# Kernel tuning notes

Hardware: AMD Instinct MI355X
Metric: run time of the kernel (lower is better)

Reference implementation:

```python
import jax, jax.numpy as jnp
import numpy as np

B, S, D = 4, 2048, 768
H = 12
DH = D // H
FF = 4 * D
EPS = 1e-5


def _layernorm(x, g, b):
    mu = jnp.mean(x, axis=-1, keepdims=True)
    var = jnp.mean(jnp.square(x - mu), axis=-1, keepdims=True)
    return (x - mu) * jax.lax.rsqrt(var + EPS) * g + b


def setup_inputs() -> dict:
    key = jax.random.key(0)
    ks = jax.random.split(key, 16)
    s_d = 1.0 / np.sqrt(D)
    s_ff = 1.0 / np.sqrt(FF)
    inp = {
        "x": jax.random.normal(ks[0], (B, S, D), jnp.float32),
        # LayerNorm 1
        "ln1_g": jnp.ones((D,), jnp.float32),
        "ln1_b": jnp.zeros((D,), jnp.float32),
        # attention linears (stored as [in, out], i.e. already transposed)
        "Wq": jax.random.normal(ks[1], (D, D), jnp.float32) * s_d,
        "bq": jax.random.normal(ks[2], (D,), jnp.float32) * s_d,
        "Wk": jax.random.normal(ks[3], (D, D), jnp.float32) * s_d,
        "bk": jax.random.normal(ks[4], (D,), jnp.float32) * s_d,
        "Wv": jax.random.normal(ks[5], (D, D), jnp.float32) * s_d,
        "bv": jax.random.normal(ks[6], (D,), jnp.float32) * s_d,
        "Wo": jax.random.normal(ks[7], (D, D), jnp.float32) * s_d,
        "bo": jax.random.normal(ks[8], (D,), jnp.float32) * s_d,
        # LayerNorm 2
        "ln2_g": jnp.ones((D,), jnp.float32),
        "ln2_b": jnp.zeros((D,), jnp.float32),
        # feed-forward (bias always on, per torch code)
        "W1": jax.random.normal(ks[9], (D, FF), jnp.float32) * s_d,
        "b1": jax.random.normal(ks[10], (FF,), jnp.float32) * s_d,
        "W2": jax.random.normal(ks[11], (FF, D), jnp.float32) * s_ff,
        "b2": jax.random.normal(ks[12], (D,), jnp.float32) * s_ff,
    }
    return inp


def reference(x, ln1_g, ln1_b, Wq, bq, Wk, bk, Wv, bv, Wo, bo,
              ln2_g, ln2_b, W1, b1, W2, b2):
    # --- attention branch (pre-LN) ---
    h = _layernorm(x, ln1_g, ln1_b)
    q = (h @ Wq + bq).reshape(B, S, H, DH).transpose(0, 2, 1, 3)  # [B,H,S,DH]
    k = (h @ Wk + bk).reshape(B, S, H, DH).transpose(0, 2, 1, 3)
    v = (h @ Wv + bv).reshape(B, S, H, DH).transpose(0, 2, 1, 3)
    scores = jnp.einsum("bhqd,bhkd->bhqk", q, k) / np.sqrt(DH)
    causal = jnp.tril(jnp.ones((S, S), bool))
    scores = jnp.where(causal, scores, -jnp.inf)
    attn = jax.nn.softmax(scores, axis=-1)
    out = jnp.einsum("bhqk,bhkd->bhqd", attn, v)
    out = out.transpose(0, 2, 1, 3).reshape(B, S, D)
    x = x + (out @ Wo + bo)
    # --- feed-forward branch (pre-LN, exact GELU) ---
    h2 = _layernorm(x, ln2_g, ln2_b)
    ff = jax.nn.gelu(h2 @ W1 + b1, approximate=False) @ W2 + b2
    return x + ff
```

## Files before the change

kernel.cpp:

```cpp
#include <hip/hip_runtime.h>
#include <math.h>

#define B_ 4
#define S_ 2048
#define D_ 768
#define H_ 12
#define DH_ 64
#define FF_ 3072

using short8  = __attribute__((ext_vector_type(8))) short;
using f32x4   = __attribute__((ext_vector_type(4))) float;
using f32x16  = __attribute__((ext_vector_type(16))) float;
using float4v = __attribute__((ext_vector_type(4))) float;
using ushort4v= __attribute__((ext_vector_type(4))) unsigned short;

__device__ __forceinline__ unsigned short f2bf(float f) {
  unsigned u = __builtin_bit_cast(unsigned, f);
  u += 0x7FFFu + ((u >> 16) & 1u);
  return (unsigned short)(u >> 16);
}

__device__ __forceinline__ unsigned cvt_pk_bf16(float a, float b) {
  unsigned r;
  asm("v_cvt_pk_bf16_f32 %0, %1, %2" : "=v"(r) : "v"(a), "v"(b));
  return r;
}

__device__ __forceinline__ void gload16(const void* g, void* l) {
  __builtin_amdgcn_global_load_lds(
      (const __attribute__((address_space(1))) unsigned*)g,
      (__attribute__((address_space(3))) unsigned*)l, 16, 0, 0);
}

__global__ __launch_bounds__(256) void transpose_cast_kernel(
    const float* __restrict__ in, unsigned short* __restrict__ out, int K, int N) {
  __shared__ float tile[32][33];
  int k0 = blockIdx.x * 32, n0 = blockIdx.y * 32;
  int tx = threadIdx.x, ty = threadIdx.y;
#pragma unroll
  for (int i = 0; i < 4; i++)
    tile[ty + 8*i][tx] = in[(size_t)(k0 + ty + 8*i) * N + n0 + tx];
  __syncthreads();
#pragma unroll
  for (int i = 0; i < 4; i++)
    out[(size_t)(n0 + ty + 8*i) * K + k0 + tx] = f2bf(tile[tx][ty + 8*i]);
}

__global__ void bias_cat_kernel(const float* __restrict__ bq, const float* __restrict__ bk,
                                const float* __restrict__ bv, float* __restrict__ dst) {
  int i = blockIdx.x * 256 + threadIdx.x;
  if (i >= 3 * D_) return;
  float v;
  if (i < D_)            v = bq[i];
  else if (i < 2 * D_)   v = bk[i - D_];
  else                   v = bv[i - 2 * D_];
  dst[i] = v;
}

__global__ __launch_bounds__(256) void layernorm_kernel(
    const float* __restrict__ x, const float* __restrict__ g,
    const float* __restrict__ b, unsigned short* __restrict__ out) {
  int wave = threadIdx.x >> 6, lane = threadIdx.x & 63;
  int row = blockIdx.x * 4 + wave;
  const float* xr = x + (size_t)row * D_;
  float4v v[3];
  float sum = 0.f, sq = 0.f;
#pragma unroll
  for (int i = 0; i < 3; i++) {
    v[i] = reinterpret_cast<const float4v*>(xr)[lane + 64*i];
#pragma unroll
    for (int j = 0; j < 4; j++) { sum += v[i][j]; sq += v[i][j]*v[i][j]; }
  }
#pragma unroll
  for (int d = 1; d < 64; d <<= 1) { sum += __shfl_xor(sum, d); sq += __shfl_xor(sq, d); }
  float mu   = sum * (1.0f / D_);
  float var  = sq  * (1.0f / D_) - mu * mu;
  float rstd = rsqrtf(var + 1e-5f);
  unsigned short* orow = out + (size_t)row * D_;
#pragma unroll
  for (int i = 0; i < 3; i++) {
    int idx = (lane + 64*i) * 4;
    ushort4v o;
#pragma unroll
    for (int j = 0; j < 4; j++)
      o[j] = f2bf((v[i][j] - mu) * rstd * g[idx + j] + b[idx + j]);
    *reinterpret_cast<ushort4v*>(orow + idx) = o;
  }
}

#define EPI_QKV   0
#define EPI_OPROJ 1
#define EPI_GELU  2
#define EPI_FINAL 3

template<int EPI>
__global__ __launch_bounds__(256) void gemm_kernel(
    const unsigned short* __restrict__ A, int lda,
    const unsigned short* __restrict__ BT, int K,
    const float* __restrict__ bias,
    const float* __restrict__ resid,
    float* __restrict__ outf,
    unsigned short* __restrict__ outh,
    int ldo, float ascale, int nN) {
  __shared__ __attribute__((aligned(16))) unsigned short As[2][128*32];
  __shared__ __attribute__((aligned(16))) unsigned short Bs[2][128*32];
  int tid = threadIdx.x;
  int wave = tid >> 6, lane = tid & 63;
  int lrow = lane & 15, lk = lane >> 4;
  int bid = blockIdx.x;
  int xcd = bid & 7, j = bid >> 3;
  int nM8 = gridDim.x / (8 * nN);
  int m0 = (xcd * nM8 + j / nN) * 128;
  int n0 = (j % nN) * 128;
  int wm = (wave >> 1) * 64, wn = (wave & 1) * 64;

  auto STAGE = [&](int buf, int k0) {
#pragma unroll
    for (int i = 0; i < 2; i++) {
      int ch = i * 256 + tid;
      int row = ch >> 2, slot = ch & 3;
      int col = k0 + 8 * (slot ^ (row & 3));
      gload16(A  + (size_t)(m0 + row) * lda + col, &As[buf][(i*256 + wave*64) * 8]);
      gload16(BT + (size_t)(n0 + row) * K   + col, &Bs[buf][(i*256 + wave*64) * 8]);
    }
  };

  f32x4 acc[4][4] = {};
  STAGE(0, 0);
  __syncthreads();
  int nt = K / 32;
  for (int t = 0; t < nt; t++) {
    int cur = t & 1;
    if (t + 1 < nt) STAGE(cur ^ 1, (t + 1) * 32);
    short8 af[4], bf[4];
#pragma unroll
    for (int mi = 0; mi < 4; mi++) {
      int row = wm + mi*16 + lrow;
      af[mi] = *reinterpret_cast<const short8*>(&As[cur][row*32 + ((lk ^ (row & 3)) * 8)]);
    }
#pragma unroll
    for (int ni = 0; ni < 4; ni++) {
      int row = wn + ni*16 + lrow;
      bf[ni] = *reinterpret_cast<const short8*>(&Bs[cur][row*32 + ((lk ^ (row & 3)) * 8)]);
    }
#pragma unroll
    for (int mi = 0; mi < 4; mi++)
#pragma unroll
      for (int ni = 0; ni < 4; ni++)
        acc[mi][ni] = __builtin_amdgcn_mfma_f32_16x16x32_bf16(af[mi], bf[ni], acc[mi][ni], 0, 0, 0);
    __syncthreads();
  }
  int pproj = (EPI == EPI_QKV) ? (n0 / D_) : 0;
#pragma unroll
  for (int mi = 0; mi < 4; mi++) {
#pragma unroll
    for (int ni = 0; ni < 4; ni++) {
#pragma unroll
      for (int r = 0; r < 4; r++) {
        int gm = m0 + wm + mi*16 + (lane >> 4)*4 + r;
        int gn = n0 + wn + ni*16 + lrow;
        float v = acc[mi][ni][r] + bias[gn];
        if constexpr (EPI == EPI_QKV) {
          if (gn < D_) v *= ascale;
          int c = gn - pproj * D_;
          size_t idx = (((size_t)(pproj*B_ + (gm >> 11)) * H_ + (c >> 6)) * S_ + (gm & 2047)) * DH_ + (c & 63);
          outh[idx] = f2bf(v);
        } else if constexpr (EPI == EPI_OPROJ) {
          size_t idx = (size_t)gm * ldo + gn;
          outf[idx] = v + resid[idx];
        } else if constexpr (EPI == EPI_GELU) {
          float gv = 0.5f * v * (1.0f + erff(v * 0.70710678118654752f));
          outh[(size_t)gm * ldo + gn] = f2bf(gv);
        } else {
          size_t idx = (size_t)gm * ldo + gn;
          outf[idx] = v + resid[idx];
        }
      }
    }
  }
}

__global__ __launch_bounds__(256) void attn_kernel(
    const unsigned short* __restrict__ q,
    const unsigned short* __restrict__ k,
    const unsigned short* __restrict__ v,
    unsigned short* __restrict__ o) {
  __shared__ __attribute__((aligned(16))) unsigned short Ks[2][64*64];
  __shared__ __attribute__((aligned(16))) unsigned short VT[2][64*64];
  __shared__ __attribute__((aligned(16))) unsigned short P2[4][32*64];
  int tid = threadIdx.x;
  int wave = tid >> 6, lane = tid & 63;
  int ql = lane & 31, hi = lane >> 5;
  int bid = blockIdx.x;
  int xcd = bid & 7, kk = bid >> 3;
  int bx = kk & 7;
  int bh = (kk >> 3) * 8 + xcd;
  const unsigned short* qb = q + (size_t)bh * S_ * DH_;
  const unsigned short* kb = k + (size_t)bh * S_ * DH_;
  const unsigned short* vb = v + (size_t)bh * S_ * DH_;
  unsigned short* Pw = P2[wave];
  int swq = (ql & 7) << 4;
  int bb = bh / H_, hh = bh % H_;

  int sr = tid >> 2;
  int sc16 = (tid & 3) * 16;
  int kp = tid & 31, dh0 = (tid >> 5) * 8;
  uint4 krA, krB, vrA, vrB;

  auto LOADR = [&](int kb0) {
    const unsigned short* ksrc = kb + (size_t)(kb0 + sr) * DH_ + sc16;
    krA = *reinterpret_cast<const uint4*>(ksrc);
    krB = *reinterpret_cast<const uint4*>(ksrc + 8);
    const unsigned short* vsrc = vb + (size_t)(kb0 + 2*kp) * DH_ + dh0;
    vrA = *reinterpret_cast<const uint4*>(vsrc);
    vrB = *reinterpret_cast<const uint4*>(vsrc + DH_);
  };
  auto WRITE = [&](int buf) {
    int sw = (sr & 7) << 4;
    int cb = sc16 * 2;
    *reinterpret_cast<uint4*>(&Ks[buf][(sr*128 + (cb ^ sw)) >> 1]) = krA;
    *reinterpret_cast<uint4*>(&Ks[buf][(sr*128 + ((cb + 16) ^ sw)) >> 1]) = krB;
    union { uint4 u4; unsigned short s[8]; } a, b;
    a.u4 = vrA; b.u4 = vrB;
#pragma unroll
    for (int j = 0; j < 8; j++) {
      int row = dh0 + j, sw2 = (row & 7) << 4;
      *reinterpret_cast<unsigned*>(&VT[buf][(row*128 + ((4*kp) ^ sw2)) >> 1]) =
          (unsigned)a.s[j] | ((unsigned)b.s[j] << 16);
    }
  };

#pragma unroll
  for (int pass = 0; pass < 2; pass++) {
    int qtile = pass ? bx : (15 - bx);
    int q0 = qtile * 128;
    int qw = q0 + wave * 32;
    int myq = qw + ql;

    short8 qf[4];
#pragma unroll
    for (int dblk = 0; dblk < 4; dblk++)
      qf[dblk] = *reinterpret_cast<const short8*>(qb + (size_t)myq * DH_ + dblk*16 + hi*8);

    f32x16 oaccT[2] = {};
    float mst = -1e30f, lst = 0.f;
    int nt = q0 / 64 + 2;

    LOADR(0);
    WRITE(0);
    __syncthreads();

    for (int kt = 0; kt < nt; kt++) {
      int kb0 = kt * 64;
      int cur = kt & 1;
      if (kt + 1 < nt) LOADR((kt + 1) * 64);

      if (kb0 <= qw + 31) {
        f32x16 sc[2] = {};
#pragma unroll
        for (int dblk = 0; dblk < 4; dblk++) {
#pragma unroll
          for (int blk = 0; blk < 2; blk++) {
            int row = blk*32 + ql;
            int sw = (row & 7) << 4;
            short8 kf = *reinterpret_cast<const short8*>(
                &Ks[cur][(row*128 + (((unsigned)(dblk*32 + hi*16)) ^ sw)) >> 1]);
            sc[blk] = __builtin_amdgcn_mfma_f32_32x32x16_bf16(kf, qf[dblk], sc[blk], 0, 0, 0);
          }
        }
        bool full = (kb0 + 63 <= qw);
        if (!full) {
#pragma unroll
          for (int blk = 0; blk < 2; blk++)
#pragma unroll
            for (int r = 0; r < 16; r++) {
              int key = kb0 + blk*32 + (r & 3) + 8*(r >> 2) + 4*hi;
              if (key > myq) sc[blk][r] = -1e30f;
            }
        }
        float pm0 = -1e30f, pm1 = -1e30f, pm2 = -1e30f, pm3 = -1e30f;
#pragma unroll
        for (int blk = 0; blk < 2; blk++)
#pragma unroll
          for (int g = 0; g < 4; g++) {
            pm0 = fmaxf(pm0, sc[blk][4*g]);
            pm1 = fmaxf(pm1, sc[blk][4*g+1]);
            pm2 = fmaxf(pm2, sc[blk][4*g+2]);
            pm3 = fmaxf(pm3, sc[blk][4*g+3]);
          }
        float mx = fmaxf(fmaxf(pm0, pm1), fmaxf(pm2, pm3));
        mx = fmaxf(mx, __shfl_xor(mx, 32));
        if (!__all(mx <= mst + 8.0f)) {
          float mnew = fmaxf(mst, mx);
          float fac = exp2f(mst - mnew);
          lst *= fac;
#pragma unroll
          for (int db = 0; db < 2; db++)
#pragma unroll
            for (int r = 0; r < 16; r++) oaccT[db][r] *= fac;
          mst = mnew;
        }
        float ps0 = 0.f, ps1 = 0.f, ps2 = 0.f, ps3 = 0.f;
#pragma unroll
        for (int blk = 0; blk < 2; blk++)
#pragma unroll
          for (int g = 0; g < 4; g++) {
            float p0 = exp2f(sc[blk][4*g]   - mst);
            float p1 = exp2f(sc[blk][4*g+1] - mst);
            float p2 = exp2f(sc[blk][4*g+2] - mst);
            float p3 = exp2f(sc[blk][4*g+3] - mst);
            ps0 += p0; ps1 += p1; ps2 += p2; ps3 += p3;
            uint2 val;
            val.x = cvt_pk_bf16(p0, p1);
            val.y = cvt_pk_bf16(p2, p3);
            int cbyte = (blk*64 + g*16 + hi*8) ^ swq;
            *reinterpret_cast<uint2*>(&Pw[(ql*128 + cbyte) >> 1]) = val;
          }
        float rs = (ps0 + ps1) + (ps2 + ps3);
        rs += __shfl_xor(rs, 32);
        lst += rs;
#pragma unroll
        for (int ks = 0; ks < 4; ks++) {
          int cb = ks*32 + hi*16;
          short8 pa = *reinterpret_cast<const short8*>(&Pw[(ql*128 + (cb ^ swq)) >> 1]);
#pragma unroll
          for (int db = 0; db < 2; db++) {
            int row = db*32 + ql;
            int sw = (row & 7) << 4;
            short8 vf = *reinterpret_cast<const short8*>(&VT[cur][(row*128 + (cb ^ sw)) >> 1]);
            oaccT[db] = __builtin_amdgcn_mfma_f32_32x32x16_bf16(vf, pa, oaccT[db], 0, 0, 0);
          }
        }
      }

      if (kt + 1 < nt) WRITE((kt + 1) & 1);
      __syncthreads();
    }

    float inv = 1.0f / lst;
    unsigned short* ob = o + ((size_t)(bb * S_ + myq)) * D_ + hh * DH_;
#pragma unroll
    for (int db = 0; db < 2; db++)
#pragma unroll
      for (int g = 0; g < 8; g++) {
        int r = 2 * g;
        int dh = db*32 + (r & 3) + 8*(r >> 2) + 4*hi;
        unsigned pk = cvt_pk_bf16(oaccT[db][r] * inv, oaccT[db][r+1] * inv);
        *reinterpret_cast<unsigned*>(ob + dh) = pk;
      }
  }
}

extern "C" void kernel_launch(void* const* d_in, const int* in_sizes, int n_in,
                              void* d_out, int out_size, void* d_ws, size_t ws_size,
                              hipStream_t stream) {
  (void)in_sizes; (void)n_in; (void)out_size; (void)ws_size;
  const float* x    = (const float*)d_in[0];
  const float* ln1g = (const float*)d_in[1];
  const float* ln1b = (const float*)d_in[2];
  const float* Wq   = (const float*)d_in[3];
  const float* bq   = (const float*)d_in[4];
  const float* Wk   = (const float*)d_in[5];
  const float* bk   = (const float*)d_in[6];
  const float* Wv   = (const float*)d_in[7];
  const float* bv   = (const float*)d_in[8];
  const float* Wo   = (const float*)d_in[9];
  const float* bo   = (const float*)d_in[10];
  const float* ln2g = (const float*)d_in[11];
  const float* ln2b = (const float*)d_in[12];
  const float* W1   = (const float*)d_in[13];
  const float* b1   = (const float*)d_in[14];
  const float* W2   = (const float*)d_in[15];
  const float* b2   = (const float*)d_in[16];
  float* out = (float*)d_out;

  char* ws = (char*)d_ws;
  size_t off = 0;
  auto alloc = [&](size_t bytes) {
    char* p = ws + off;
    off += (bytes + 255) & ~(size_t)255;
    return p;
  };
  unsigned short* WqT = (unsigned short*)alloc((size_t)D_*D_*2);
  unsigned short* WkT = (unsigned short*)alloc((size_t)D_*D_*2);
  unsigned short* WvT = (unsigned short*)alloc((size_t)D_*D_*2);
  unsigned short* WoT = (unsigned short*)alloc((size_t)D_*D_*2);
  unsigned short* W1T = (unsigned short*)alloc((size_t)D_*FF_*2);
  unsigned short* W2T = (unsigned short*)alloc((size_t)FF_*D_*2);
  unsigned short* h   = (unsigned short*)alloc((size_t)B_*S_*D_*2);
  unsigned short* qb  = (unsigned short*)alloc((size_t)B_*S_*D_*2);
  unsigned short* kbf = (unsigned short*)alloc((size_t)B_*S_*D_*2);
  unsigned short* vbf = (unsigned short*)alloc((size_t)B_*S_*D_*2);
  unsigned short* ob  = (unsigned short*)alloc((size_t)B_*S_*D_*2);
  float* bias_cat     = (float*)alloc((size_t)3*D_*4);
  unsigned short* ffb = qb;
  unsigned short* h2  = h;

  const float qscale = 0.125f * 1.4426950408889634f;

  dim3 tb(32, 8);
  transpose_cast_kernel<<<dim3(D_/32,  D_/32),  tb, 0, stream>>>(Wq, WqT, D_,  D_);
  transpose_cast_kernel<<<dim3(D_/32,  D_/32),  tb, 0, stream>>>(Wk, WkT, D_,  D_);
  transpose_cast_kernel<<<dim3(D_/32,  D_/32),  tb, 0, stream>>>(Wv, WvT, D_,  D_);
  transpose_cast_kernel<<<dim3(D_/32,  D_/32),  tb, 0, stream>>>(Wo, WoT, D_,  D_);
  transpose_cast_kernel<<<dim3(D_/32,  FF_/32), tb, 0, stream>>>(W1, W1T, D_,  FF_);
  transpose_cast_kernel<<<dim3(FF_/32, D_/32),  tb, 0, stream>>>(W2, W2T, FF_, D_);
  bias_cat_kernel<<<9, 256, 0, stream>>>(bq, bk, bv, bias_cat);

  layernorm_kernel<<<(B_*S_)/4, 256, 0, stream>>>(x, ln1g, ln1b, h);

  gemm_kernel<EPI_QKV><<<dim3(64*18), 256, 0, stream>>>(
      h, D_, WqT, D_, bias_cat, nullptr, nullptr, qb, D_, qscale, 18);

  attn_kernel<<<dim3(384), 256, 0, stream>>>(qb, kbf, vbf, ob);

  gemm_kernel<EPI_OPROJ><<<dim3(64*6), 256, 0, stream>>>(
      ob, D_, WoT, D_, bo, x, out, nullptr, D_, 1.0f, 6);

  layernorm_kernel<<<(B_*S_)/4, 256, 0, stream>>>(out, ln2g, ln2b, h2);

  gemm_kernel<EPI_GELU><<<dim3(64*24), 256, 0, stream>>>(
      h2, D_, W1T, D_, b1, nullptr, nullptr, ffb, FF_, 1.0f, 24);

  gemm_kernel<EPI_FINAL><<<dim3(64*6), 256, 0, stream>>>(
      ffb, FF_, W2T, FF_, b2, out, out, nullptr, D_, 1.0f, 6);
}
```

Baseline: 321.9 us.

## Triple-buffer GEMM, write interleaved QKV, split attention passes, merge weight casts

```diff
diff --git a/kernel.cpp b/kernel.cpp
--- a/kernel.cpp
+++ b/kernel.cpp
@@ -7,6 +7,7 @@
 #define H_ 12
 #define DH_ 64
 #define FF_ 3072
+#define LDQ (3*D_)
 
 using short8  = __attribute__((ext_vector_type(8))) short;
 using f32x4   = __attribute__((ext_vector_type(4))) float;
@@ -32,10 +33,27 @@
       (__attribute__((address_space(3))) unsigned*)l, 16, 0, 0);
 }
 
-__global__ __launch_bounds__(256) void transpose_cast_kernel(
-    const float* __restrict__ in, unsigned short* __restrict__ out, int K, int N) {
+__global__ __launch_bounds__(256) void transpose_cast_multi_kernel(
+    const float* __restrict__ Wq, const float* __restrict__ Wk,
+    const float* __restrict__ Wv, const float* __restrict__ Wo,
+    const float* __restrict__ W1, const float* __restrict__ W2,
+    unsigned short* __restrict__ WqT, unsigned short* __restrict__ WkT,
+    unsigned short* __restrict__ WvT, unsigned short* __restrict__ WoT,
+    unsigned short* __restrict__ W1T, unsigned short* __restrict__ W2T) {
   __shared__ float tile[32][33];
-  int k0 = blockIdx.x * 32, n0 = blockIdx.y * 32;
+  int bid = blockIdx.x;
+  const float* in; unsigned short* out; int K, N, t;
+  if (bid < 2304) {
+    int seg = bid / 576; t = bid % 576; K = D_; N = D_;
+    in  = seg == 0 ? Wq  : seg == 1 ? Wk  : seg == 2 ? Wv  : Wo;
+    out = seg == 0 ? WqT : seg == 1 ? WkT : seg == 2 ? WvT : WoT;
+  } else if (bid < 4608) {
+    t = bid - 2304; K = D_; N = FF_; in = W1; out = W1T;
+  } else {
+    t = bid - 4608; K = FF_; N = D_; in = W2; out = W2T;
+  }
+  int ntk = K / 32;
+  int k0 = (t % ntk) * 32, n0 = (t / ntk) * 32;
   int tx = threadIdx.x, ty = threadIdx.y;
 #pragma unroll
   for (int i = 0; i < 4; i++)
@@ -102,8 +120,7 @@
     float* __restrict__ outf,
     unsigned short* __restrict__ outh,
     int ldo, float ascale, int nN) {
-  __shared__ __attribute__((aligned(16))) unsigned short As[2][128*32];
-  __shared__ __attribute__((aligned(16))) unsigned short Bs[2][128*32];
+  __shared__ __attribute__((aligned(16))) unsigned short Ls[3][128*64];
   int tid = threadIdx.x;
   int wave = tid >> 6, lane = tid & 63;
   int lrow = lane & 15, lk = lane >> 4;
@@ -116,41 +133,46 @@
 
   auto STAGE = [&](int buf, int k0) {
 #pragma unroll
-    for (int i = 0; i < 2; i++) {
+    for (int i = 0; i < 4; i++) {
       int ch = i * 256 + tid;
-      int row = ch >> 2, slot = ch & 3;
-      int col = k0 + 8 * (slot ^ (row & 3));
-      gload16(A  + (size_t)(m0 + row) * lda + col, &As[buf][(i*256 + wave*64) * 8]);
-      gload16(BT + (size_t)(n0 + row) * K   + col, &Bs[buf][(i*256 + wave*64) * 8]);
+      int row = ch >> 3, s8 = ch & 7;
+      int m = s8 ^ (row & 7);
+      const unsigned short* src = (m < 4)
+        ? A  + (size_t)(m0 + row) * lda + k0 + m * 8
+        : BT + (size_t)(n0 + row) * K   + k0 + (m - 4) * 8;
+      gload16(src, &Ls[buf][(i*256 + wave*64) * 8]);
     }
   };
 
   f32x4 acc[4][4] = {};
+  int nt = K / 32;
   STAGE(0, 0);
-  __syncthreads();
-  int nt = K / 32;
+  STAGE(1, 32);
   for (int t = 0; t < nt; t++) {
-    int cur = t & 1;
-    if (t + 1 < nt) STAGE(cur ^ 1, (t + 1) * 32);
+    if (t + 1 < nt) { asm volatile("s_waitcnt vmcnt(4)" ::: "memory"); }
+    else            { asm volatile("s_waitcnt vmcnt(0)" ::: "memory"); }
+    __builtin_amdgcn_s_barrier();
+    const unsigned short* Lc = Ls[t % 3];
     short8 af[4], bf[4];
 #pragma unroll
     for (int mi = 0; mi < 4; mi++) {
       int row = wm + mi*16 + lrow;
-      af[mi] = *reinterpret_cast<const short8*>(&As[cur][row*32 + ((lk ^ (row & 3)) * 8)]);
+      af[mi] = *reinterpret_cast<const short8*>(&Lc[row*64 + ((lk ^ (row & 7)) * 8)]);
     }
 #pragma unroll
     for (int ni = 0; ni < 4; ni++) {
       int row = wn + ni*16 + lrow;
-      bf[ni] = *reinterpret_cast<const short8*>(&Bs[cur][row*32 + ((lk ^ (row & 3)) * 8)]);
-    }
+      bf[ni] = *reinterpret_cast<const short8*>(&Lc[row*64 + (((4 + lk) ^ (row & 7)) * 8)]);
+    }
+    if (t + 2 < nt) STAGE((t + 2) % 3, (t + 2) * 32);
+    __builtin_amdgcn_s_setprio(1);
 #pragma unroll
     for (int mi = 0; mi < 4; mi++)
 #pragma unroll
       for (int ni = 0; ni < 4; ni++)
         acc[mi][ni] = __builtin_amdgcn_mfma_f32_16x16x32_bf16(af[mi], bf[ni], acc[mi][ni], 0, 0, 0);
-    __syncthreads();
-  }
-  int pproj = (EPI == EPI_QKV) ? (n0 / D_) : 0;
+    __builtin_amdgcn_s_setprio(0);
+  }
 #pragma unroll
   for (int mi = 0; mi < 4; mi++) {
 #pragma unroll
@@ -162,9 +184,7 @@
         float v = acc[mi][ni][r] + bias[gn];
         if constexpr (EPI == EPI_QKV) {
           if (gn < D_) v *= ascale;
-          int c = gn - pproj * D_;
-          size_t idx = (((size_t)(pproj*B_ + (gm >> 11)) * H_ + (c >> 6)) * S_ + (gm & 2047)) * DH_ + (c & 63);
-          outh[idx] = f2bf(v);
+          outh[(size_t)gm * ldo + gn] = f2bf(v);
         } else if constexpr (EPI == EPI_OPROJ) {
           size_t idx = (size_t)gm * ldo + gn;
           outf[idx] = v + resid[idx];
@@ -181,9 +201,7 @@
 }
 
 __global__ __launch_bounds__(256) void attn_kernel(
-    const unsigned short* __restrict__ q,
-    const unsigned short* __restrict__ k,
-    const unsigned short* __restrict__ v,
+    const unsigned short* __restrict__ qkv,
     unsigned short* __restrict__ o) {
   __shared__ __attribute__((aligned(16))) unsigned short Ks[2][64*64];
   __shared__ __attribute__((aligned(16))) unsigned short VT[2][64*64];
@@ -192,15 +210,15 @@
   int wave = tid >> 6, lane = tid & 63;
   int ql = lane & 31, hi = lane >> 5;
   int bid = blockIdx.x;
-  int xcd = bid & 7, kk = bid >> 3;
-  int bx = kk & 7;
-  int bh = (kk >> 3) * 8 + xcd;
-  const unsigned short* qb = q + (size_t)bh * S_ * DH_;
-  const unsigned short* kb = k + (size_t)bh * S_ * DH_;
-  const unsigned short* vb = v + (size_t)bh * S_ * DH_;
+  int xcd = bid & 7, r = bid >> 3;
+  int bh = xcd * 6 + (r % 6);
+  int qtile = 15 - (r / 6);
+  int bb = bh / H_, hh = bh % H_;
+  const unsigned short* qb = qkv + (size_t)bb * S_ * LDQ + hh * DH_;
+  const unsigned short* kb = qb + D_;
+  const unsigned short* vb = qb + 2 * D_;
   unsigned short* Pw = P2[wave];
   int swq = (ql & 7) << 4;
-  int bb = bh / H_, hh = bh % H_;
 
   int sr = tid >> 2;
   int sc16 = (tid & 3) * 16;
@@ -208,12 +226,12 @@
   uint4 krA, krB, vrA, vrB;
 
   auto LOADR = [&](int kb0) {
-    const unsigned short* ksrc = kb + (size_t)(kb0 + sr) * DH_ + sc16;
+    const unsigned short* ksrc = kb + (size_t)(kb0 + sr) * LDQ + sc16;
     krA = *reinterpret_cast<const uint4*>(ksrc);
     krB = *reinterpret_cast<const uint4*>(ksrc + 8);
-    const unsigned short* vsrc = vb + (size_t)(kb0 + 2*kp) * DH_ + dh0;
+    const unsigned short* vsrc = vb + (size_t)(kb0 + 2*kp) * LDQ + dh0;
     vrA = *reinterpret_cast<const uint4*>(vsrc);
-    vrB = *reinterpret_cast<const uint4*>(vsrc + DH_);
+    vrB = *reinterpret_cast<const uint4*>(vsrc + LDQ);
   };
   auto WRITE = [&](int buf) {
     int sw = (sr & 7) << 4;
@@ -223,132 +241,132 @@
     union { uint4 u4; unsigned short s[8]; } a, b;
     a.u4 = vrA; b.u4 = vrB;
 #pragma unroll
-    for (int j = 0; j < 8; j++) {
-      int row = dh0 + j, sw2 = (row & 7) << 4;
+    for (int j2 = 0; j2 < 8; j2++) {
+      int row = dh0 + j2, sw2 = (row & 7) << 4;
       *reinterpret_cast<unsigned*>(&VT[buf][(row*128 + ((4*kp) ^ sw2)) >> 1]) =
-          (unsigned)a.s[j] | ((unsigned)b.s[j] << 16);
+          (unsigned)a.s[j2] | ((unsigned)b.s[j2] << 16);
     }
   };
 
-#pragma unroll
-  for (int pass = 0; pass < 2; pass++) {
-    int qtile = pass ? bx : (15 - bx);
-    int q0 = qtile * 128;
-    int qw = q0 + wave * 32;
-    int myq = qw + ql;
-
-    short8 qf[4];
-#pragma unroll
-    for (int dblk = 0; dblk < 4; dblk++)
-      qf[dblk] = *reinterpret_cast<const short8*>(qb + (size_t)myq * DH_ + dblk*16 + hi*8);
-
-    f32x16 oaccT[2] = {};
-    float mst = -1e30f, lst = 0.f;
-    int nt = q0 / 64 + 2;
-
-    LOADR(0);
-    WRITE(0);
-    __syncthreads();
-
-    for (int kt = 0; kt < nt; kt++) {
-      int kb0 = kt * 64;
-      int cur = kt & 1;
-      if (kt + 1 < nt) LOADR((kt + 1) * 64);
-
-      if (kb0 <= qw + 31) {
-        f32x16 sc[2] = {};
-#pragma unroll
-        for (int dblk = 0; dblk < 4; dblk++) {
-#pragma unroll
-          for (int blk = 0; blk < 2; blk++) {
-            int row = blk*32 + ql;
-            int sw = (row & 7) << 4;
-            short8 kf = *reinterpret_cast<const short8*>(
-                &Ks[cur][(row*128 + (((unsigned)(dblk*32 + hi*16)) ^ sw)) >> 1]);
-            sc[blk] = __builtin_amdgcn_mfma_f32_32x32x16_bf16(kf, qf[dblk], sc[blk], 0, 0, 0);
-          }
-        }
-        bool full = (kb0 + 63 <= qw);
-        if (!full) {
-#pragma unroll
-          for (int blk = 0; blk < 2; blk++)
-#pragma unroll
-            for (int r = 0; r < 16; r++) {
-              int key = kb0 + blk*32 + (r & 3) + 8*(r >> 2) + 4*hi;
-              if (key > myq) sc[blk][r] = -1e30f;
-            }
-        }
-        float pm0 = -1e30f, pm1 = -1e30f, pm2 = -1e30f, pm3 = -1e30f;
-#pragma unroll
-        for (int blk = 0; blk < 2; blk++)
-#pragma unroll
-          for (int g = 0; g < 4; g++) {
-            pm0 = fmaxf(pm0, sc[blk][4*g]);
-            pm1 = fmaxf(pm1, sc[blk][4*g+1]);
-            pm2 = fmaxf(pm2, sc[blk][4*g+2]);
-            pm3 = fmaxf(pm3, sc[blk][4*g+3]);
-          }
-        float mx = fmaxf(fmaxf(pm0, pm1), fmaxf(pm2, pm3));
-        mx = fmaxf(mx, __shfl_xor(mx, 32));
-        if (!__all(mx <= mst + 8.0f)) {
-          float mnew = fmaxf(mst, mx);
-          float fac = exp2f(mst - mnew);
-          lst *= fac;
-#pragma unroll
-          for (int db = 0; db < 2; db++)
-#pragma unroll
-            for (int r = 0; r < 16; r++) oaccT[db][r] *= fac;
-          mst = mnew;
-        }
-        float ps0 = 0.f, ps1 = 0.f, ps2 = 0.f, ps3 = 0.f;
-#pragma unroll
-        for (int blk = 0; blk < 2; blk++)
-#pragma unroll
-          for (int g = 0; g < 4; g++) {
-            float p0 = exp2f(sc[blk][4*g]   - mst);
-            float p1 = exp2f(sc[blk][4*g+1] - mst);
-            float p2 = exp2f(sc[blk][4*g+2] - mst);
-            float p3 = exp2f(sc[blk][4*g+3] - mst);
-            ps0 += p0; ps1 += p1; ps2 += p2; ps3 += p3;
-            uint2 val;
-            val.x = cvt_pk_bf16(p0, p1);
-            val.y = cvt_pk_bf16(p2, p3);
-            int cbyte = (blk*64 + g*16 + hi*8) ^ swq;
-            *reinterpret_cast<uint2*>(&Pw[(ql*128 + cbyte) >> 1]) = val;
-          }
-        float rs = (ps0 + ps1) + (ps2 + ps3);
-        rs += __shfl_xor(rs, 32);
-        lst += rs;
-#pragma unroll
-        for (int ks = 0; ks < 4; ks++) {
-          int cb = ks*32 + hi*16;
-          short8 pa = *reinterpret_cast<const short8*>(&Pw[(ql*128 + (cb ^ swq)) >> 1]);
-#pragma unroll
-          for (int db = 0; db < 2; db++) {
-            int row = db*32 + ql;
-            int sw = (row & 7) << 4;
-            short8 vf = *reinterpret_cast<const short8*>(&VT[cur][(row*128 + (cb ^ sw)) >> 1]);
-            oaccT[db] = __builtin_amdgcn_mfma_f32_32x32x16_bf16(vf, pa, oaccT[db], 0, 0, 0);
-          }
+  int q0 = qtile * 128;
+  int qw = q0 + wave * 32;
+  int myq = qw + ql;
+
+  short8 qf[4];
+#pragma unroll
+  for (int dblk = 0; dblk < 4; dblk++)
+    qf[dblk] = *reinterpret_cast<const short8*>(qb + (size_t)myq * LDQ + dblk*16 + hi*8);
+
+  f32x16 oaccT[2] = {};
+  float mst = -1e30f, lst = 0.f;
+  int nt = q0 / 64 + 2;
+
+  LOADR(0);
+  WRITE(0);
+  __syncthreads();
+
+  for (int kt = 0; kt < nt; kt++) {
+    int kb0 = kt * 64;
+    int cur = kt & 1;
+    if (kt + 1 < nt) LOADR((kt + 1) * 64);
+
+    if (kb0 <= qw + 31) {
+      f32x16 sc[2] = {};
+      __builtin_amdgcn_s_setprio(1);
+#pragma unroll
+      for (int dblk = 0; dblk < 4; dblk++) {
+#pragma unroll
+        for (int blk = 0; blk < 2; blk++) {
+          int row = blk*32 + ql;
+          int sw = (row & 7) << 4;
+          short8 kf = *reinterpret_cast<const short8*>(
+              &Ks[cur][(row*128 + (((unsigned)(dblk*32 + hi*16)) ^ sw)) >> 1]);
+          sc[blk] = __builtin_amdgcn_mfma_f32_32x32x16_bf16(kf, qf[dblk], sc[blk], 0, 0, 0);
         }
       }
-
-      if (kt + 1 < nt) WRITE((kt + 1) & 1);
-      __syncthreads();
-    }
-
-    float inv = 1.0f / lst;
-    unsigned short* ob = o + ((size_t)(bb * S_ + myq)) * D_ + hh * DH_;
-#pragma unroll
-    for (int db = 0; db < 2; db++)
-#pragma unroll
-      for (int g = 0; g < 8; g++) {
-        int r = 2 * g;
-        int dh = db*32 + (r & 3) + 8*(r >> 2) + 4*hi;
-        unsigned pk = cvt_pk_bf16(oaccT[db][r] * inv, oaccT[db][r+1] * inv);
-        *reinterpret_cast<unsigned*>(ob + dh) = pk;
+      __builtin_amdgcn_s_setprio(0);
+      bool full = (kb0 + 63 <= qw);
+      if (!full) {
+#pragma unroll
+        for (int blk = 0; blk < 2; blk++)
+#pragma unroll
+          for (int r2 = 0; r2 < 16; r2++) {
+            int key = kb0 + blk*32 + (r2 & 3) + 8*(r2 >> 2) + 4*hi;
+            if (key > myq) sc[blk][r2] = -1e30f;
+          }
       }
-  }
+      float pm0 = -1e30f, pm1 = -1e30f, pm2 = -1e30f, pm3 = -1e30f;
+#pragma unroll
+      for (int blk = 0; blk < 2; blk++)
+#pragma unroll
+        for (int g = 0; g < 4; g++) {
+          pm0 = fmaxf(pm0, sc[blk][4*g]);
+          pm1 = fmaxf(pm1, sc[blk][4*g+1]);
+          pm2 = fmaxf(pm2, sc[blk][4*g+2]);
+          pm3 = fmaxf(pm3, sc[blk][4*g+3]);
+        }
+      float mx = fmaxf(fmaxf(pm0, pm1), fmaxf(pm2, pm3));
+      mx = fmaxf(mx, __shfl_xor(mx, 32));
+      if (!__all(mx <= mst + 8.0f)) {
+        float mnew = fmaxf(mst, mx);
+        float fac = exp2f(mst - mnew);
+        lst *= fac;
+#pragma unroll
+        for (int db = 0; db < 2; db++)
+#pragma unroll
+          for (int r2 = 0; r2 < 16; r2++) oaccT[db][r2] *= fac;
+        mst = mnew;
+      }
+      float ps0 = 0.f, ps1 = 0.f, ps2 = 0.f, ps3 = 0.f;
+#pragma unroll
+      for (int blk = 0; blk < 2; blk++)
+#pragma unroll
+        for (int g = 0; g < 4; g++) {
+          float p0 = exp2f(sc[blk][4*g]   - mst);
+          float p1 = exp2f(sc[blk][4*g+1] - mst);
+          float p2 = exp2f(sc[blk][4*g+2] - mst);
+          float p3 = exp2f(sc[blk][4*g+3] - mst);
+          ps0 += p0; ps1 += p1; ps2 += p2; ps3 += p3;
+          uint2 val;
+          val.x = cvt_pk_bf16(p0, p1);
+          val.y = cvt_pk_bf16(p2, p3);
+          int cbyte = (blk*64 + g*16 + hi*8) ^ swq;
+          *reinterpret_cast<uint2*>(&Pw[(ql*128 + cbyte) >> 1]) = val;
+        }
+      float rs = (ps0 + ps1) + (ps2 + ps3);
+      rs += __shfl_xor(rs, 32);
+      lst += rs;
+      __builtin_amdgcn_s_setprio(1);
+#pragma unroll
+      for (int ks = 0; ks < 4; ks++) {
+        int cb = ks*32 + hi*16;
+        short8 pa = *reinterpret_cast<const short8*>(&Pw[(ql*128 + (cb ^ swq)) >> 1]);
+#pragma unroll
+        for (int db = 0; db < 2; db++) {
+          int row = db*32 + ql;
+          int sw = (row & 7) << 4;
+          short8 vf = *reinterpret_cast<const short8*>(&VT[cur][(row*128 + (cb ^ sw)) >> 1]);
+          oaccT[db] = __builtin_amdgcn_mfma_f32_32x32x16_bf16(vf, pa, oaccT[db], 0, 0, 0);
+        }
+      }
+      __builtin_amdgcn_s_setprio(0);
+    }
+
+    if (kt + 1 < nt) WRITE((kt + 1) & 1);
+    __syncthreads();
+  }
+
+  float inv = 1.0f / lst;
+  unsigned short* ob = o + ((size_t)(bb * S_ + myq)) * D_ + hh * DH_;
+#pragma unroll
+  for (int db = 0; db < 2; db++)
+#pragma unroll
+    for (int g = 0; g < 8; g++) {
+      int r2 = 2 * g;
+      int dh = db*32 + (r2 & 3) + 8*(r2 >> 2) + 4*hi;
+      unsigned pk = cvt_pk_bf16(oaccT[db][r2] * inv, oaccT[db][r2+1] * inv);
+      *reinterpret_cast<unsigned*>(ob + dh) = pk;
+    }
 }
 
 extern "C" void kernel_launch(void* const* d_in, const int* in_sizes, int n_in,
@@ -388,31 +406,25 @@
   unsigned short* W1T = (unsigned short*)alloc((size_t)D_*FF_*2);
   unsigned short* W2T = (unsigned short*)alloc((size_t)FF_*D_*2);
   unsigned short* h   = (unsigned short*)alloc((size_t)B_*S_*D_*2);
-  unsigned short* qb  = (unsigned short*)alloc((size_t)B_*S_*D_*2);
-  unsigned short* kbf = (unsigned short*)alloc((size_t)B_*S_*D_*2);
-  unsigned short* vbf = (unsigned short*)alloc((size_t)B_*S_*D_*2);
+  unsigned short* qkv = (unsigned short*)alloc((size_t)B_*S_*LDQ*2);
   unsigned short* ob  = (unsigned short*)alloc((size_t)B_*S_*D_*2);
   float* bias_cat     = (float*)alloc((size_t)3*D_*4);
-  unsigned short* ffb = qb;
+  unsigned short* ffb = qkv;
   unsigned short* h2  = h;
 
   const float qscale = 0.125f * 1.4426950408889634f;
 
   dim3 tb(32, 8);
-  transpose_cast_kernel<<<dim3(D_/32,  D_/32),  tb, 0, stream>>>(Wq, WqT, D_,  D_);
-  transpose_cast_kernel<<<dim3(D_/32,  D_/32),  tb, 0, stream>>>(Wk, WkT, D_,  D_);
-  transpose_cast_kernel<<<dim3(D_/32,  D_/32),  tb, 0, stream>>>(Wv, WvT, D_,  D_);
-  transpose_cast_kernel<<<dim3(D_/32,  D_/32),  tb, 0, stream>>>(Wo, WoT, D_,  D_);
-  transpose_cast_kernel<<<dim3(D_/32,  FF_/32), tb, 0, stream>>>(W1, W1T, D_,  FF_);
-  transpose_cast_kernel<<<dim3(FF_/32, D_/32),  tb, 0, stream>>>(W2, W2T, FF_, D_);
+  transpose_cast_multi_kernel<<<6912, tb, 0, stream>>>(
+      Wq, Wk, Wv, Wo, W1, W2, WqT, WkT, WvT, WoT, W1T, W2T);
   bias_cat_kernel<<<9, 256, 0, stream>>>(bq, bk, bv, bias_cat);
 
   layernorm_kernel<<<(B_*S_)/4, 256, 0, stream>>>(x, ln1g, ln1b, h);
 
   gemm_kernel<EPI_QKV><<<dim3(64*18), 256, 0, stream>>>(
-      h, D_, WqT, D_, bias_cat, nullptr, nullptr, qb, D_, qscale, 18);
-
-  attn_kernel<<<dim3(384), 256, 0, stream>>>(qb, kbf, vbf, ob);
+      h, D_, WqT, D_, bias_cat, nullptr, nullptr, qkv, LDQ, qscale, 18);
+
+  attn_kernel<<<dim3(768), 256, 0, stream>>>(qkv, ob);
 
   gemm_kernel<EPI_OPROJ><<<dim3(64*6), 256, 0, stream>>>(
       ob, D_, WoT, D_, bo, x, out, nullptr, D_, 1.0f, 6);
```

After: 278.3 us. -13.5%, faster.
